# Optimization experiments

Hardware: AMD Instinct MI355X
Metric: run time of the kernel (lower is better)

## Reference

```python
import jax, jax.numpy as jnp
import numpy as np

B, T, D, H = 2, 2048, 1024, 16
DK = D // H

def setup_inputs() -> dict:
    key = jax.random.key(0)
    ks = jax.random.split(key, 12)
    s = 1.0 / np.sqrt(D)
    inp = {
        'Q': jax.random.normal(ks[0], (B, T, D), jnp.float32),
        'K': jax.random.normal(ks[1], (B, T, D), jnp.float32),
        'V': jax.random.normal(ks[2], (B, T, D), jnp.float32),
        'mask': jnp.tril(jnp.ones((T, T), jnp.int32))[None, None],  # causal [1,1,T,T]
        'Wq_w': jax.random.normal(ks[3], (D, D), jnp.float32) * s,
        'Wq_b': jax.random.normal(ks[4], (D,), jnp.float32) * s,
        'Wk_w': jax.random.normal(ks[5], (D, D), jnp.float32) * s,
        'Wk_b': jax.random.normal(ks[6], (D,), jnp.float32) * s,
        'Wv_w': jax.random.normal(ks[7], (D, D), jnp.float32) * s,
        'Wv_b': jax.random.normal(ks[8], (D,), jnp.float32) * s,
        'Wo_w': jax.random.normal(ks[9], (D, D), jnp.float32) * s,
        'Wo_b': jax.random.normal(ks[10], (D,), jnp.float32) * s,
    }
    return inp

def reference(Q, K, V, mask, Wq_w, Wq_b, Wk_w, Wk_b, Wv_w, Wv_b, Wo_w, Wo_b):
    b, tq, c = Q.shape
    tk = K.shape[1]
    q = (Q @ Wq_w + Wq_b).reshape(b, tq, H, DK).transpose(0, 2, 1, 3)  # [B,H,Tq,dk]
    k = (K @ Wk_w + Wk_b).reshape(b, tk, H, DK).transpose(0, 2, 1, 3)
    v = (V @ Wv_w + Wv_b).reshape(b, tk, H, DK).transpose(0, 2, 1, 3)
    scores = jnp.einsum('bhqd,bhkd->bhqk', q, k) / jnp.sqrt(jnp.float32(DK))
    scores = jnp.where(mask == 0, jnp.float32(-1e9), scores)
    attn = jax.nn.softmax(scores, axis=-1)
    out = jnp.einsum('bhqk,bhkd->bhqd', attn, v)
    out = out.transpose(0, 2, 1, 3).reshape(b, tq, c)
    return out @ Wo_w + Wo_b
```

## Files before the change

kernel.cpp:

```cpp
#include <hip/hip_runtime.h>
#include <hip/hip_bf16.h>

#define NB 2
#define NT 2048
#define ND 1024
#define NH 16
#define NDK 64

typedef __attribute__((ext_vector_type(8))) short bf16x8;
typedef __attribute__((ext_vector_type(4))) float f32x4;

static __device__ __forceinline__ short f2bf(float f) {
  union { float f; unsigned u; } c; c.f = f;
  unsigned u = c.u;
  u += 0x7FFF + ((u >> 16) & 1);
  return (short)(u >> 16);
}

static __device__ __forceinline__ unsigned cvt_pk_bf16(float lo, float hi) {
  unsigned r;
  asm("v_cvt_pk_bf16_f32 %0, %1, %2" : "=v"(r) : "v"(lo), "v"(hi));
  return r;
}

static __device__ __forceinline__ void gload16(const void* g, void* l) {
  __builtin_amdgcn_global_load_lds((const __attribute__((address_space(1))) void*)g,
                                   (__attribute__((address_space(3))) void*)l, 16, 0, 0);
}

__global__ void cast3_kernel(const float* __restrict__ s0, const float* __restrict__ s1,
                             const float* __restrict__ s2,
                             short* __restrict__ t0, short* __restrict__ t1,
                             short* __restrict__ t2) {
  int z = blockIdx.x >> 11;
  int i = (blockIdx.x & 2047) * 256 + threadIdx.x;
  const float* src = z == 0 ? s0 : (z == 1 ? s1 : s2);
  short* dst       = z == 0 ? t0 : (z == 1 ? t1 : t2);
  const float4* s4 = (const float4*)src + (size_t)i * 2;
  float4 a = s4[0], b = s4[1];
  bf16x8 o;
  o[0] = f2bf(a.x); o[1] = f2bf(a.y); o[2] = f2bf(a.z); o[3] = f2bf(a.w);
  o[4] = f2bf(b.x); o[5] = f2bf(b.y); o[6] = f2bf(b.z); o[7] = f2bf(b.w);
  *((bf16x8*)dst + i) = o;
}

__global__ void wtrans_kernel(const float* __restrict__ W0, const float* __restrict__ W1,
                              const float* __restrict__ W2, const float* __restrict__ W3,
                              short* __restrict__ T0, short* __restrict__ T1,
                              short* __restrict__ T2, short* __restrict__ T3) {
  __shared__ float t[32][33];
  int z = blockIdx.z;
  const float* W = z == 0 ? W0 : (z == 1 ? W1 : (z == 2 ? W2 : W3));
  short* Wt      = z == 0 ? T0 : (z == 1 ? T1 : (z == 2 ? T2 : T3));
  int n0 = blockIdx.x * 32, k0 = blockIdx.y * 32;
  int tx = threadIdx.x, ty = threadIdx.y;
  for (int i = ty; i < 32; i += 8) t[i][tx] = W[(size_t)(k0 + i) * ND + n0 + tx];
  __syncthreads();
  for (int i = ty; i < 32; i += 8) Wt[(size_t)(n0 + i) * ND + k0 + tx] = f2bf(t[tx][i]);
}

template <int MODE>
__global__ __launch_bounds__(256, 2) void gemm_bt(
    const short* __restrict__ A0, const short* __restrict__ A1, const short* __restrict__ A2,
    const short* __restrict__ W0, const short* __restrict__ W1, const short* __restrict__ W2,
    const float* __restrict__ b0, const float* __restrict__ b1, const float* __restrict__ b2,
    void* o0, void* o1, void* o2)
{
  constexpr int K = ND;
  __shared__ short As[2][128 * 32];
  __shared__ short Bs[2][128 * 32];
  int z = blockIdx.z;
  const short* A    = z == 0 ? A0 : (z == 1 ? A1 : A2);
  const short* Wt   = z == 0 ? W0 : (z == 1 ? W1 : W2);
  const float* bias = z == 0 ? b0 : (z == 1 ? b1 : b2);
  void* out         = z == 0 ? o0 : (z == 1 ? o1 : o2);
  float scl = (MODE == 0 && z == 0) ? 0.18033688011112042f : 1.0f;

  int m0 = blockIdx.y * 128, n0 = blockIdx.x * 128;
  int tid = threadIdx.x, wid = tid >> 6, lane = tid & 63;
  int wr = wid >> 1, wc = wid & 1;
  int r16 = lane & 15, l4 = lane >> 4;

  auto stage = [&](int buf, int kt) {
    int rbase = wid * 32;
    int row = rbase + (lane >> 2);
    int c8 = (lane & 3) * 8;
    const short* ga = A  + (size_t)(m0 + row) * K + kt * 32 + c8;
    const short* gb = Wt + (size_t)(n0 + row) * K + kt * 32 + c8;
    gload16(ga,          &As[buf][rbase * 32]);
    gload16(ga + 16 * K, &As[buf][(rbase + 16) * 32]);
    gload16(gb,          &Bs[buf][rbase * 32]);
    gload16(gb + 16 * K, &Bs[buf][(rbase + 16) * 32]);
  };

  f32x4 acc[4][4] = {};
  stage(0, 0);
  __syncthreads();

  for (int kt = 0; kt < K / 32; ++kt) {
    int cur = kt & 1;
    if (kt + 1 < K / 32) stage(cur ^ 1, kt + 1);
    bf16x8 af[4], bfv[4];
    int kk = l4 * 8;
#pragma unroll
    for (int mi = 0; mi < 4; mi++)
      af[mi] = *(const bf16x8*)&As[cur][(wr * 64 + mi * 16 + r16) * 32 + kk];
#pragma unroll
    for (int ni = 0; ni < 4; ni++)
      bfv[ni] = *(const bf16x8*)&Bs[cur][(wc * 64 + ni * 16 + r16) * 32 + kk];
#pragma unroll
    for (int mi = 0; mi < 4; mi++)
#pragma unroll
      for (int ni = 0; ni < 4; ni++)
        acc[mi][ni] = __builtin_amdgcn_mfma_f32_16x16x32_bf16(af[mi], bfv[ni], acc[mi][ni], 0, 0, 0);
    __syncthreads();
  }

  int mb = m0 + wr * 64, nb = n0 + wc * 64;
#pragma unroll
  for (int mi = 0; mi < 4; mi++)
#pragma unroll
    for (int ni = 0; ni < 4; ni++) {
      int n = nb + ni * 16 + r16;
      float bv = bias[n];
      if constexpr (MODE == 0) {
        int h = n >> 6, dk = n & 63;
        if (z == 2) {
          int m0_ = mb + mi * 16 + l4 * 4;
          int bI = m0_ >> 11, t0 = m0_ & (NT - 1);
          int bh = bI * NH + h;
          short4 s4;
          s4.x = f2bf(acc[mi][ni][0] + bv);
          s4.y = f2bf(acc[mi][ni][1] + bv);
          s4.z = f2bf(acc[mi][ni][2] + bv);
          s4.w = f2bf(acc[mi][ni][3] + bv);
          *(short4*)&((short*)out)[(size_t)bh * 131072 + (dk >> 4) * 32768 +
                                   (t0 >> 3) * 128 + (dk & 15) * 8 + (t0 & 7)] = s4;
        } else if (z == 1) {
#pragma unroll
          for (int r = 0; r < 4; r++) {
            int m = mb + mi * 16 + l4 * 4 + r;
            int bI = m >> 11, t = m & (NT - 1);
            int bh = bI * NH + h;
            ((short*)out)[(size_t)bh * 131072 + (t >> 4) * 1024 + (dk >> 3) * 128 +
                          (t & 15) * 8 + (dk & 7)] = f2bf(acc[mi][ni][r] + bv);
          }
        } else {
#pragma unroll
          for (int r = 0; r < 4; r++) {
            int m = mb + mi * 16 + l4 * 4 + r;
            int bI = m >> 11, t = m & (NT - 1);
            ((short*)out)[((((size_t)bI * NH + h) * NT + t) << 6) + dk] = f2bf((acc[mi][ni][r] + bv) * scl);
          }
        }
      } else {
#pragma unroll
        for (int r = 0; r < 4; r++) {
          int m = mb + mi * 16 + l4 * 4 + r;
          ((float*)out)[(size_t)m * ND + n] = acc[mi][ni][r] + bv;
        }
      }
    }
}

__global__ __launch_bounds__(256) void attn_kernel(
    const short* __restrict__ q, const short* __restrict__ k, const short* __restrict__ vt,
    short* __restrict__ O)
{
  struct SH {
    union {
      short p2[4][2][16][72];
      struct {
        f32x4 obuf[4][2][2][64];
        float ol[4][32];
      } mg;
    };
  };
  __shared__ SH sh;

  int d = blockIdx.x;
  int xcd = d & 7, jj = d >> 3;
  int bh = xcd * 4 + (jj >> 6);
  int qg = 63 - (jj & 63);
  int b = bh >> 4, h = bh & 15;
  int tid = threadIdx.x, wid = tid >> 6, lane = tid & 63;
  int r16 = lane & 15, l4 = lane >> 4;
  size_t hb = (size_t)bh * NT * NDK;
  const short* qh = q + hb;
  const short* kh = k + hb;
  const short* vh = vt + hb;
  int qw = qg * 32;

  bf16x8 qa[2][2];
#pragma unroll
  for (int rf = 0; rf < 2; rf++)
#pragma unroll
    for (int kf = 0; kf < 2; kf++)
      qa[rf][kf] = *(const bf16x8*)(qh + (size_t)(qw + rf * 16 + r16) * NDK + kf * 32 + l4 * 8);

  f32x4 of[2][4] = {};
  float l_[2] = { 0.f, 0.f };

  int nt = (qw + 95) >> 6;
  for (int kt = wid; kt < nt; kt += 4) {
    int kv0 = kt * 64;

    f32x4 sf[2][4] = {};
    __builtin_amdgcn_s_setprio(1);
#pragma unroll
    for (int cf = 0; cf < 4; cf++) {
      const short* kb_ = kh + (size_t)((kv0 >> 4) + cf) * 1024 + lane * 8;
      bf16x8 k0 = *(const bf16x8*)kb_;
      bf16x8 k1 = *(const bf16x8*)(kb_ + 512);
      sf[0][cf] = __builtin_amdgcn_mfma_f32_16x16x32_bf16(k0, qa[0][0], sf[0][cf], 0, 0, 0);
      sf[1][cf] = __builtin_amdgcn_mfma_f32_16x16x32_bf16(k0, qa[1][0], sf[1][cf], 0, 0, 0);
      sf[0][cf] = __builtin_amdgcn_mfma_f32_16x16x32_bf16(k1, qa[0][1], sf[0][cf], 0, 0, 0);
      sf[1][cf] = __builtin_amdgcn_mfma_f32_16x16x32_bf16(k1, qa[1][1], sf[1][cf], 0, 0, 0);
    }
    __builtin_amdgcn_s_setprio(0);

    bf16x8 vb[4][2];
#pragma unroll
    for (int df = 0; df < 4; df++)
#pragma unroll
      for (int kf = 0; kf < 2; kf++)
        vb[df][kf] = *(const bf16x8*)(vh + df * 32768 + (kv0 >> 3) * 128 + kf * 512 + lane * 8);

    if (kv0 + 63 > qw) {
#pragma unroll
      for (int rf = 0; rf < 2; rf++)
#pragma unroll
        for (int cf = 0; cf < 4; cf++)
#pragma unroll
          for (int r = 0; r < 4; r++) {
            int kvi = kv0 + cf * 16 + l4 * 4 + r;
            int qi = qw + rf * 16 + r16;
            if (kvi > qi) sf[rf][cf][r] = -1e30f;
          }
    }

#pragma unroll
    for (int rf = 0; rf < 2; rf++) {
      float rs = 0.f;
#pragma unroll
      for (int cf = 0; cf < 4; cf++) {
        float p0 = __builtin_amdgcn_exp2f(sf[rf][cf][0]);
        float p1 = __builtin_amdgcn_exp2f(sf[rf][cf][1]);
        float p2v = __builtin_amdgcn_exp2f(sf[rf][cf][2]);
        float p3 = __builtin_amdgcn_exp2f(sf[rf][cf][3]);
        rs += (p0 + p1) + (p2v + p3);
        unsigned w0 = cvt_pk_bf16(p0, p1);
        unsigned w1 = cvt_pk_bf16(p2v, p3);
        *(int2*)&sh.p2[wid][rf][r16][cf * 16 + l4 * 4] = make_int2((int)w0, (int)w1);
      }
      l_[rf] += rs;
    }

    __builtin_amdgcn_s_setprio(1);
#pragma unroll
    for (int rf = 0; rf < 2; rf++)
#pragma unroll
      for (int kf = 0; kf < 2; kf++) {
        bf16x8 pa = *(const bf16x8*)&sh.p2[wid][rf][r16][kf * 32 + l4 * 8];
#pragma unroll
        for (int df = 0; df < 4; df++)
          of[rf][df] = __builtin_amdgcn_mfma_f32_16x16x32_bf16(vb[df][kf], pa, of[rf][df], 0, 0, 0);
      }
    __builtin_amdgcn_s_setprio(0);
  }

#pragma unroll
  for (int rf = 0; rf < 2; rf++) {
    float t = l_[rf];
    t += __shfl_xor(t, 16);
    t += __shfl_xor(t, 32);
    l_[rf] = t;
  }

  __syncthreads();
  if (l4 == 0) {
    sh.mg.ol[wid][r16] = l_[0];
    sh.mg.ol[wid][16 + r16] = l_[1];
  }
#pragma unroll
  for (int pass = 0; pass < 2; ++pass) {
#pragma unroll
    for (int rf = 0; rf < 2; rf++)
#pragma unroll
      for (int dfp = 0; dfp < 2; dfp++)
        sh.mg.obuf[wid][rf][dfp][lane] = of[rf][2 * pass + dfp];
    __syncthreads();
    {
      int mrf = wid >> 1, mdfp = wid & 1, mdf = 2 * pass + mdfp;
      int row = mrf * 16 + r16;
      float lst = sh.mg.ol[0][row] + sh.mg.ol[1][row] + sh.mg.ol[2][row] + sh.mg.ol[3][row];
      float rinv = 1.0f / lst;
      f32x4 o0 = sh.mg.obuf[0][mrf][mdfp][lane];
      f32x4 o1 = sh.mg.obuf[1][mrf][mdfp][lane];
      f32x4 o2 = sh.mg.obuf[2][mrf][mdfp][lane];
      f32x4 o3 = sh.mg.obuf[3][mrf][mdfp][lane];
      float v0 = (o0[0] + o1[0] + o2[0] + o3[0]) * rinv;
      float v1 = (o0[1] + o1[1] + o2[1] + o3[1]) * rinv;
      float v2 = (o0[2] + o1[2] + o2[2] + o3[2]) * rinv;
      float v3 = (o0[3] + o1[3] + o2[3] + o3[3]) * rinv;
      int t = qw + mrf * 16 + r16;
      *(int2*)&O[(size_t)(b * NT + t) * ND + h * 64 + mdf * 16 + l4 * 4] =
          make_int2((int)cvt_pk_bf16(v0, v1), (int)cvt_pk_bf16(v2, v3));
    }
    __syncthreads();
  }
}

extern "C" void kernel_launch(void* const* d_in, const int* in_sizes, int n_in,
                              void* d_out, int out_size, void* d_ws, size_t ws_size,
                              hipStream_t stream)
{
  const float* Q  = (const float*)d_in[0];
  const float* Ki = (const float*)d_in[1];
  const float* V  = (const float*)d_in[2];
  const float* Wq = (const float*)d_in[4];  const float* bq = (const float*)d_in[5];
  const float* Wk = (const float*)d_in[6];  const float* bk = (const float*)d_in[7];
  const float* Wv = (const float*)d_in[8];  const float* bv = (const float*)d_in[9];
  const float* Wo = (const float*)d_in[10]; const float* bo = (const float*)d_in[11];

  short* ws = (short*)d_ws;
  const size_t M4 = (size_t)4 * 1024 * 1024;
  short* Qb  = ws;
  short* Kb  = ws + M4;
  short* Vb  = ws + 2 * M4;
  short* qp  = ws + 3 * M4;
  short* kp  = ws + 4 * M4;
  short* vtp = ws + 5 * M4;
  short* Wqt = ws + 6 * M4;
  short* Wkt = Wqt + 1024 * 1024;
  short* Wvt = Wkt + 1024 * 1024;
  short* Wot = Wvt + 1024 * 1024;
  short* Obuf = Qb;

  cast3_kernel<<<6144, 256, 0, stream>>>(Q, Ki, V, Qb, Kb, Vb);
  wtrans_kernel<<<dim3(32, 32, 4), dim3(32, 8), 0, stream>>>(Wq, Wk, Wv, Wo,
                                                             Wqt, Wkt, Wvt, Wot);

  gemm_bt<0><<<dim3(8, 32, 3), 256, 0, stream>>>(Qb, Kb, Vb, Wqt, Wkt, Wvt,
                                                 bq, bk, bv, qp, kp, vtp);
  attn_kernel<<<2048, 256, 0, stream>>>(qp, kp, vtp, Obuf);
  gemm_bt<1><<<dim3(8, 32, 1), 256, 0, stream>>>(Obuf, Obuf, Obuf, Wot, Wot, Wot,
                                                 bo, bo, bo, d_out, d_out, d_out);
}
```

Measured before the change: 132.1 us.

## Prefetch next K tile in attention and narrow output GEMM tile to 64 columns

In the attention kernel the K fragments for the next tile each wave processes are loaded into registers right after the current QK MFMAs. This hides global-load latency behind softmax and PV work, at the cost of extra VGPRs. The output-projection GEMM is templated on BN and now runs with 128x64 tiles on a 16x32 grid instead of 8x32. That doubles its block count to 512 so more CUs are busy, but each block reuses its A tile less.

```diff
diff --git a/kernel.cpp b/kernel.cpp
--- a/kernel.cpp
+++ b/kernel.cpp
@@ -59,7 +59,7 @@
   for (int i = ty; i < 32; i += 8) Wt[(size_t)(n0 + i) * ND + k0 + tx] = f2bf(t[tx][i]);
 }
 
-template <int MODE>
+template <int MODE, int BN>
 __global__ __launch_bounds__(256, 2) void gemm_bt(
     const short* __restrict__ A0, const short* __restrict__ A1, const short* __restrict__ A2,
     const short* __restrict__ W0, const short* __restrict__ W1, const short* __restrict__ W2,
@@ -67,8 +67,9 @@
     void* o0, void* o1, void* o2)
 {
   constexpr int K = ND;
+  constexpr int NI = BN / 32;
   __shared__ short As[2][128 * 32];
-  __shared__ short Bs[2][128 * 32];
+  __shared__ short Bs[2][BN * 32];
   int z = blockIdx.z;
   const short* A    = z == 0 ? A0 : (z == 1 ? A1 : A2);
   const short* Wt   = z == 0 ? W0 : (z == 1 ? W1 : W2);
@@ -76,51 +77,60 @@
   void* out         = z == 0 ? o0 : (z == 1 ? o1 : o2);
   float scl = (MODE == 0 && z == 0) ? 0.18033688011112042f : 1.0f;
 
-  int m0 = blockIdx.y * 128, n0 = blockIdx.x * 128;
+  int m0 = blockIdx.y * 128, n0 = blockIdx.x * BN;
   int tid = threadIdx.x, wid = tid >> 6, lane = tid & 63;
   int wr = wid >> 1, wc = wid & 1;
   int r16 = lane & 15, l4 = lane >> 4;
 
   auto stage = [&](int buf, int kt) {
-    int rbase = wid * 32;
-    int row = rbase + (lane >> 2);
+    int row = (lane >> 2);
     int c8 = (lane & 3) * 8;
-    const short* ga = A  + (size_t)(m0 + row) * K + kt * 32 + c8;
-    const short* gb = Wt + (size_t)(n0 + row) * K + kt * 32 + c8;
-    gload16(ga,          &As[buf][rbase * 32]);
-    gload16(ga + 16 * K, &As[buf][(rbase + 16) * 32]);
-    gload16(gb,          &Bs[buf][rbase * 32]);
-    gload16(gb + 16 * K, &Bs[buf][(rbase + 16) * 32]);
+    {
+      int rbase = wid * 32;
+      const short* ga = A + (size_t)(m0 + rbase + row) * K + kt * 32 + c8;
+      gload16(ga,          &As[buf][rbase * 32]);
+      gload16(ga + 16 * K, &As[buf][(rbase + 16) * 32]);
+    }
+    if constexpr (BN == 128) {
+      int rbase = wid * 32;
+      const short* gb = Wt + (size_t)(n0 + rbase + row) * K + kt * 32 + c8;
+      gload16(gb,          &Bs[buf][rbase * 32]);
+      gload16(gb + 16 * K, &Bs[buf][(rbase + 16) * 32]);
+    } else {
+      int rbase = wid * 16;
+      const short* gb = Wt + (size_t)(n0 + rbase + row) * K + kt * 32 + c8;
+      gload16(gb,          &Bs[buf][rbase * 32]);
+    }
   };
 
-  f32x4 acc[4][4] = {};
+  f32x4 acc[4][NI] = {};
   stage(0, 0);
   __syncthreads();
 
   for (int kt = 0; kt < K / 32; ++kt) {
     int cur = kt & 1;
     if (kt + 1 < K / 32) stage(cur ^ 1, kt + 1);
-    bf16x8 af[4], bfv[4];
+    bf16x8 af[4], bfv[NI];
     int kk = l4 * 8;
 #pragma unroll
     for (int mi = 0; mi < 4; mi++)
       af[mi] = *(const bf16x8*)&As[cur][(wr * 64 + mi * 16 + r16) * 32 + kk];
 #pragma unroll
-    for (int ni = 0; ni < 4; ni++)
-      bfv[ni] = *(const bf16x8*)&Bs[cur][(wc * 64 + ni * 16 + r16) * 32 + kk];
+    for (int ni = 0; ni < NI; ni++)
+      bfv[ni] = *(const bf16x8*)&Bs[cur][(wc * (BN / 2) + ni * 16 + r16) * 32 + kk];
 #pragma unroll
     for (int mi = 0; mi < 4; mi++)
 #pragma unroll
-      for (int ni = 0; ni < 4; ni++)
+      for (int ni = 0; ni < NI; ni++)
         acc[mi][ni] = __builtin_amdgcn_mfma_f32_16x16x32_bf16(af[mi], bfv[ni], acc[mi][ni], 0, 0, 0);
     __syncthreads();
   }
 
-  int mb = m0 + wr * 64, nb = n0 + wc * 64;
+  int mb = m0 + wr * 64, nb = n0 + wc * (BN / 2);
 #pragma unroll
   for (int mi = 0; mi < 4; mi++)
 #pragma unroll
-    for (int ni = 0; ni < 4; ni++) {
+    for (int ni = 0; ni < NI; ni++) {
       int n = nb + ni * 16 + r16;
       float bv = bias[n];
       if constexpr (MODE == 0) {
@@ -202,6 +212,17 @@
   float l_[2] = { 0.f, 0.f };
 
   int nt = (qw + 95) >> 6;
+
+  bf16x8 kfr[4][2];
+  if (wid < nt) {
+#pragma unroll
+    for (int cf = 0; cf < 4; cf++) {
+      const short* kb_ = kh + (size_t)((wid * 64 >> 4) + cf) * 1024 + lane * 8;
+      kfr[cf][0] = *(const bf16x8*)kb_;
+      kfr[cf][1] = *(const bf16x8*)(kb_ + 512);
+    }
+  }
+
   for (int kt = wid; kt < nt; kt += 4) {
     int kv0 = kt * 64;
 
@@ -209,15 +230,23 @@
     __builtin_amdgcn_s_setprio(1);
 #pragma unroll
     for (int cf = 0; cf < 4; cf++) {
-      const short* kb_ = kh + (size_t)((kv0 >> 4) + cf) * 1024 + lane * 8;
-      bf16x8 k0 = *(const bf16x8*)kb_;
-      bf16x8 k1 = *(const bf16x8*)(kb_ + 512);
-      sf[0][cf] = __builtin_amdgcn_mfma_f32_16x16x32_bf16(k0, qa[0][0], sf[0][cf], 0, 0, 0);
-      sf[1][cf] = __builtin_amdgcn_mfma_f32_16x16x32_bf16(k0, qa[1][0], sf[1][cf], 0, 0, 0);
-      sf[0][cf] = __builtin_amdgcn_mfma_f32_16x16x32_bf16(k1, qa[0][1], sf[0][cf], 0, 0, 0);
-      sf[1][cf] = __builtin_amdgcn_mfma_f32_16x16x32_bf16(k1, qa[1][1], sf[1][cf], 0, 0, 0);
+      sf[0][cf] = __builtin_amdgcn_mfma_f32_16x16x32_bf16(kfr[cf][0], qa[0][0], sf[0][cf], 0, 0, 0);
+      sf[1][cf] = __builtin_amdgcn_mfma_f32_16x16x32_bf16(kfr[cf][0], qa[1][0], sf[1][cf], 0, 0, 0);
+      sf[0][cf] = __builtin_amdgcn_mfma_f32_16x16x32_bf16(kfr[cf][1], qa[0][1], sf[0][cf], 0, 0, 0);
+      sf[1][cf] = __builtin_amdgcn_mfma_f32_16x16x32_bf16(kfr[cf][1], qa[1][1], sf[1][cf], 0, 0, 0);
     }
     __builtin_amdgcn_s_setprio(0);
+
+    {
+      int ktn = (kt + 4 < nt) ? kt + 4 : kt;
+      int kvn = ktn * 64;
+#pragma unroll
+      for (int cf = 0; cf < 4; cf++) {
+        const short* kb_ = kh + (size_t)((kvn >> 4) + cf) * 1024 + lane * 8;
+        kfr[cf][0] = *(const bf16x8*)kb_;
+        kfr[cf][1] = *(const bf16x8*)(kb_ + 512);
+      }
+    }
 
     bf16x8 vb[4][2];
 #pragma unroll
@@ -341,9 +370,9 @@
   wtrans_kernel<<<dim3(32, 32, 4), dim3(32, 8), 0, stream>>>(Wq, Wk, Wv, Wo,
                                                              Wqt, Wkt, Wvt, Wot);
 
-  gemm_bt<0><<<dim3(8, 32, 3), 256, 0, stream>>>(Qb, Kb, Vb, Wqt, Wkt, Wvt,
-                                                 bq, bk, bv, qp, kp, vtp);
+  gemm_bt<0, 128><<<dim3(8, 32, 3), 256, 0, stream>>>(Qb, Kb, Vb, Wqt, Wkt, Wvt,
+                                                      bq, bk, bv, qp, kp, vtp);
   attn_kernel<<<2048, 256, 0, stream>>>(qp, kp, vtp, Obuf);
-  gemm_bt<1><<<dim3(8, 32, 1), 256, 0, stream>>>(Obuf, Obuf, Obuf, Wot, Wot, Wot,
-                                                 bo, bo, bo, d_out, d_out, d_out);
-}
+  gemm_bt<1, 64><<<dim3(16, 32, 1), 256, 0, stream>>>(Obuf, Obuf, Obuf, Wot, Wot, Wot,
+                                                      bo, bo, bo, d_out, d_out, d_out);
+}
```

New measurement: 125.9 us. 4.7% less time.
